# Kernel optimization log

Hardware: AMD Instinct MI355X
Metric: run time of the kernel (lower is better)

## Reference

```python
import jax, jax.numpy as jnp
import numpy as np

B, S, H, G, W = 4, 4096, 1024, 256, 8
CHUNK = 1024
NUM_HEADS = 4


def _ln(x, g, b, eps=1e-5):
    m = jnp.mean(x, axis=-1, keepdims=True)
    v = jnp.var(x, axis=-1, keepdims=True)
    return (x - m) / jnp.sqrt(v + eps) * g + b


def setup_inputs() -> dict:
    key = jax.random.key(0)
    ks = jax.random.split(key, 16)
    Hm = H // 2
    return {
        "x": jax.random.normal(ks[0], (B, S, H), dtype=jnp.float32),
        # wavelet params
        "mother_wavelets": jax.random.normal(ks[1], (1, W, H, 1), dtype=jnp.float32) * 0.02,
        "scales": jnp.ones((1, W, 1, 1), dtype=jnp.float32),
        # coeff_mixer: Linear(W,H/2) -> LN -> GELU -> Linear(H/2,H)  (weights stored as (in,out))
        "mix_w1": jax.random.normal(ks[2], (W, Hm), dtype=jnp.float32) * 0.02,
        "mix_b1": jnp.zeros((Hm,), dtype=jnp.float32),
        "mix_ln_g": jnp.ones((Hm,), dtype=jnp.float32),
        "mix_ln_b": jnp.zeros((Hm,), dtype=jnp.float32),
        "mix_w2": jax.random.normal(ks[3], (Hm, H), dtype=jnp.float32) * 0.02,
        "mix_b2": jnp.zeros((H,), dtype=jnp.float32),
        # attention (no bias)
        "wq": jax.random.normal(ks[4], (H, H), dtype=jnp.float32) * 0.02,
        "wk": jax.random.normal(ks[5], (H, H), dtype=jnp.float32) * 0.02,
        "wv": jax.random.normal(ks[6], (H, H), dtype=jnp.float32) * 0.02,
        "wo": jax.random.normal(ks[7], (H, H), dtype=jnp.float32) * 0.02,
        # output_proj: LN -> Linear(H, G)
        "out_ln_g": jnp.ones((H,), dtype=jnp.float32),
        "out_ln_b": jnp.zeros((H,), dtype=jnp.float32),
        "out_w": jax.random.normal(ks[8], (H, G), dtype=jnp.float32) * 0.02,
        "out_b": jnp.zeros((G,), dtype=jnp.float32),
    }


def reference(x, mother_wavelets, scales, mix_w1, mix_b1, mix_ln_g, mix_ln_b,
              mix_w2, mix_b2, wq, wk, wv, wo, out_ln_g, out_ln_b, out_w, out_b):
    b, s, h = x.shape
    nc = s // CHUNK  # chunks are independent -> fold into batch
    xc = x.reshape(b * nc, CHUNK, h)

    # wavelet coeffs: conv1d with kernel length == channels reduces to a dot product
    norm = jnp.sqrt(jnp.sum(mother_wavelets ** 2, axis=2, keepdims=True))
    kern = (mother_wavelets / jnp.maximum(norm, 1e-12)) * jax.nn.sigmoid(scales)
    kern = kern[0, :, :, 0]  # (W, H)
    coeffs = jnp.einsum('bsh,wh->bsw', xc, kern)  # (b*nc, L, W)

    # coeff mixer
    hid = _ln(coeffs @ mix_w1 + mix_b1, mix_ln_g, mix_ln_b)
    mixed = jax.nn.gelu(hid, approximate=False) @ mix_w2 + mix_b2  # (b*nc, L, H)

    # multi-head attention within each chunk (eval mode -> no causal mask)
    hd = h // NUM_HEADS
    def heads(t):
        return t.reshape(-1, CHUNK, NUM_HEADS, hd).transpose(0, 2, 1, 3)
    q, k, v = heads(mixed @ wq), heads(mixed @ wk), heads(mixed @ wv)
    scores = jnp.einsum('bhqd,bhkd->bhqk', q, k) * (hd ** -0.5)
    attn = jax.nn.softmax(scores, axis=-1)
    o = jnp.einsum('bhqk,bhkd->bhqd', attn, v)
    o = o.transpose(0, 2, 1, 3).reshape(-1, CHUNK, h) @ wo

    # output projection with residual
    y = _ln(o + mixed, out_ln_g, out_ln_b) @ out_w + out_b  # (b*nc, L, G)
    return y.reshape(b, s, -1)
```

## Files before the change

kernel.cpp:

```cpp
#include <hip/hip_runtime.h>
#include <hip/hip_bf16.h>

typedef __bf16 bf16;
typedef __bf16 bf16x4 __attribute__((ext_vector_type(4)));
typedef __bf16 bf16x8 __attribute__((ext_vector_type(8)));
typedef float f32x4 __attribute__((ext_vector_type(4)));
typedef unsigned short ushort8_t __attribute__((ext_vector_type(8)));
typedef unsigned int u32x2 __attribute__((ext_vector_type(2)));

#define GLOAD_LDS16(g, l)                                                      \
    __builtin_amdgcn_global_load_lds(                                          \
        (const __attribute__((address_space(1))) void*)(g),                    \
        (__attribute__((address_space(3))) void*)(l), 16, 0, 0)

#define LDS_ADDR(p) ((unsigned)(uintptr_t)(__attribute__((address_space(3))) void*)(p))

#define SBAR()                                                                 \
    do {                                                                       \
        __builtin_amdgcn_sched_barrier(0);                                     \
        __builtin_amdgcn_s_barrier();                                          \
        __builtin_amdgcn_sched_barrier(0);                                     \
    } while (0)


__global__ __launch_bounds__(256) void k_wavelet(const float* __restrict__ mw,
                                                 const float* __restrict__ sc,
                                                 float* __restrict__ kern) {
    int w = blockIdx.x;
    int tid = threadIdx.x;
    float s = 0.f;
    for (int h = tid; h < 1024; h += 256) { float v = mw[w * 1024 + h]; s += v * v; }
#pragma unroll
    for (int xm = 1; xm < 64; xm <<= 1) s += __shfl_xor(s, xm);
    __shared__ float red[4];
    if ((tid & 63) == 0) red[tid >> 6] = s;
    __syncthreads();
    float tot = red[0] + red[1] + red[2] + red[3];
    float inv = 1.f / fmaxf(sqrtf(tot), 1e-12f);
    float sg = 1.f / (1.f + __expf(-sc[w]));
    float m = inv * sg;
    for (int h = tid; h < 1024; h += 256) kern[w * 1024 + h] = mw[w * 1024 + h] * m;
}

__global__ __launch_bounds__(256) void k_coeffs(const float* __restrict__ x,
                                                const float* __restrict__ kern,
                                                float* __restrict__ coeffs) {
    __shared__ float kl[8 * 1024];
    int tid = threadIdx.x;
    for (int i = tid; i < 8192; i += 256) kl[i] = kern[i];
    __syncthreads();
    int wid = tid >> 6, lane = tid & 63;
    long row = (long)blockIdx.x * 4 + wid;
    float acc[8] = {0, 0, 0, 0, 0, 0, 0, 0};
    const float* xr = x + row * 1024;
    for (int i = 0; i < 16; i++) {
        float xv = xr[lane + i * 64];
#pragma unroll
        for (int w = 0; w < 8; w++) acc[w] += xv * kl[w * 1024 + lane + i * 64];
    }
#pragma unroll
    for (int xm = 1; xm < 64; xm <<= 1) {
#pragma unroll
        for (int w = 0; w < 8; w++) acc[w] += __shfl_xor(acc[w], xm);
    }
    if (lane == 0) {
#pragma unroll
        for (int w = 0; w < 8; w++) coeffs[row * 8 + w] = acc[w];
    }
}

__global__ __launch_bounds__(256) void k_mix1(const float* __restrict__ coeffs,
                                              const float* __restrict__ w1,
                                              const float* __restrict__ b1,
                                              const float* __restrict__ lng,
                                              const float* __restrict__ lnb,
                                              bf16* __restrict__ g) {
    long row = blockIdx.x;
    int tid = threadIdx.x;
    int wid = tid >> 6, lane = tid & 63;
    __shared__ float cf[8];
    __shared__ float red1[4], red2[4];
    if (tid < 8) cf[tid] = coeffs[row * 8 + tid];
    __syncthreads();
    float h0[2];
#pragma unroll
    for (int t = 0; t < 2; t++) {
        int j = tid + t * 256;
        float a = b1[j];
#pragma unroll
        for (int w = 0; w < 8; w++) a += cf[w] * w1[w * 512 + j];
        h0[t] = a;
    }
    float s1 = h0[0] + h0[1];
    float s2 = h0[0] * h0[0] + h0[1] * h0[1];
#pragma unroll
    for (int xm = 1; xm < 64; xm <<= 1) {
        s1 += __shfl_xor(s1, xm);
        s2 += __shfl_xor(s2, xm);
    }
    if (lane == 0) { red1[wid] = s1; red2[wid] = s2; }
    __syncthreads();
    s1 = red1[0] + red1[1] + red1[2] + red1[3];
    s2 = red2[0] + red2[1] + red2[2] + red2[3];
    float mean = s1 * (1.f / 512.f);
    float var = s2 * (1.f / 512.f) - mean * mean;
    float inv = rsqrtf(var + 1e-5f);
#pragma unroll
    for (int t = 0; t < 2; t++) {
        int j = tid + t * 256;
        float xn = (h0[t] - mean) * inv * lng[j] + lnb[j];
        float ge = 0.5f * xn * (1.f + erff(xn * 0.70710678118654752f));
        g[row * 512 + j] = (bf16)ge;
    }
}

__global__ void k_wtrans_all(const float* __restrict__ w2, const float* __restrict__ wq,
                             const float* __restrict__ wk, const float* __restrict__ wv,
                             const float* __restrict__ wo, const float* __restrict__ ow,
                             bf16* __restrict__ w2t, bf16* __restrict__ wqt,
                             bf16* __restrict__ wkt, bf16* __restrict__ wvt,
                             bf16* __restrict__ wot, bf16* __restrict__ owt) {
    long idx = (long)blockIdx.x * 256 + threadIdx.x;
    if (idx < 524288) {
        int kk = (int)(idx >> 10), n = (int)(idx & 1023);
        w2t[(long)n * 512 + kk] = (bf16)w2[idx];
    } else if (idx < 4718592) {
        long r = idx - 524288;
        int m = (int)(r >> 20);
        long q = r & 1048575;
        int kk = (int)(q >> 10), n = (int)(q & 1023);
        const float* src = (m == 0) ? wq : (m == 1) ? wk : (m == 2) ? wv : wo;
        bf16* dst = (m == 0) ? wqt : (m == 1) ? wkt : (m == 2) ? wvt : wot;
        dst[(long)n * 1024 + kk] = (bf16)src[q];
    } else {
        long r = idx - 4718592;
        int kk = (int)(r >> 8), n = (int)(r & 255);
        owt[(long)n * 1024 + kk] = (bf16)ow[r];
    }
}

enum { EPI_BF16 = 0, EPI_BF16_BIAS = 1, EPI_F32_BIAS = 2, EPI_VT = 3, EPI_F32 = 4 };

template <int EPI>
__global__ __launch_bounds__(512, 2) void k_gemm8p(const bf16* __restrict__ A,
                                                   const bf16* __restrict__ Bt,
                                                   const float* __restrict__ bias,
                                                   void* __restrict__ Cout,
                                                   int K, int lda, int ldb, int ldc,
                                                   float scale) {
    __shared__ bf16 As[2 * 2 * 128 * 64];
    __shared__ bf16 Bs[2 * 2 * 128 * 64];
    const int tid = threadIdx.x;
    const int wid = tid >> 6, lane = tid & 63;
    const int wr = wid >> 2, wc = wid & 3;
    const long m0 = (long)blockIdx.y * 256, n0 = (long)blockIdx.x * 256;
    f32x4 acc[8][4] = {};
    const int lr = lane & 15, gq = lane >> 4;
    const int l7 = lr & 7;

    const int srow = wid * 8 + (lane >> 3);
    const int sg = (lane & 7) ^ (lane >> 3);
    const bf16* aS = A + (m0 + srow) * lda + sg * 8;
    const bf16* bS = Bt + (n0 + srow) * ldb + sg * 8;

    auto stageA = [&](int t, int h) {
        bf16* d = As + (((t & 1) * 2 + h) * 128) * 64 + wid * 512;
        const long kq = (long)t << 6;
        GLOAAD_DUMMY:;
        GLOAD_LDS16(aS + (long)(h * 128) * lda + kq, d);
        GLOAD_LDS16(aS + (long)(h * 128 + 64) * lda + kq, d + 4096);
    };
    auto stageB = [&](int t, int h) {
        bf16* d = Bs + (((t & 1) * 2 + h) * 128) * 64 + wid * 512;
        const long kq = (long)t << 6;
        GLOAD_LDS16(bS + (long)(h * 128) * ldb + kq, d);
        GLOAD_LDS16(bS + (long)(h * 128 + 64) * ldb + kq, d + 4096);
    };

    bf16x8 bfr[4][2];
    auto ldB = [&](int b) {
#pragma unroll
        for (int j = 0; j < 4; j++)
#pragma unroll
            for (int kk = 0; kk < 2; kk++)
                bfr[j][kk] = *(const bf16x8*)&Bs[((b * 2 + (wc >> 1)) * 128 +
                                                 (wc & 1) * 64 + j * 16 + lr) * 64 +
                                                (((kk * 4 + gq) ^ l7) << 3)];
    };

    const int nt = K >> 6;
    const int niter = nt >> 1;

    stageA(0, 0); stageA(0, 1); stageB(0, 0); stageB(0, 1);
    stageB(1, 0); stageB(1, 1);
    asm volatile("s_waitcnt vmcnt(4)" ::: "memory");
    SBAR();

    for (int jit = 0; jit < niter - 1; ++jit) {
        const int T = jit << 1;
#pragma unroll
        for (int tp = 0; tp < 2; ++tp) {
#pragma unroll
            for (int q = 0; q < 4; ++q) {
                bf16x8 af[2][2];
                if (q == 0) ldB(tp);
#pragma unroll
                for (int ii = 0; ii < 2; ii++)
#pragma unroll
                    for (int kk = 0; kk < 2; kk++)
                        af[ii][kk] = *(const bf16x8*)&As[((tp * 2 + wr) * 128 +
                                                         (q * 2 + ii) * 16 + lr) * 64 +
                                                        (((kk * 4 + gq) ^ l7) << 3)];
                if (tp == 0) {
                    if (q == 0) stageA(T + 1, 0);
                    else if (q == 1) stageA(T + 1, 1);
                    else if (q == 2) stageB(T + 2, 0);
                    else stageB(T + 2, 1);
                } else {
                    if (q == 0) stageA(T + 2, 0);
                    else if (q == 1) stageA(T + 2, 1);
                    else if (q == 2) stageB(T + 3, 0);
                    else stageB(T + 3, 1);
                }
                if (q == 3) asm volatile("s_waitcnt vmcnt(4)" ::: "memory");
                SBAR();
                asm volatile("s_waitcnt lgkmcnt(0)" ::: "memory");
                __builtin_amdgcn_s_setprio(1);
#pragma unroll
                for (int ii = 0; ii < 2; ii++)
#pragma unroll
                    for (int j = 0; j < 4; j++) {
                        acc[q * 2 + ii][j] = __builtin_amdgcn_mfma_f32_16x16x32_bf16(
                            af[ii][0], bfr[j][0], acc[q * 2 + ii][j], 0, 0, 0);
                        acc[q * 2 + ii][j] = __builtin_amdgcn_mfma_f32_16x16x32_bf16(
                            af[ii][1], bfr[j][1], acc[q * 2 + ii][j], 0, 0, 0);
                    }
                __builtin_amdgcn_s_setprio(0);
                SBAR();
            }
        }
    }
    {
        const int T = nt - 2;
#pragma unroll
        for (int tp = 0; tp < 2; ++tp) {
#pragma unroll
            for (int q = 0; q < 4; ++q) {
                bf16x8 af[2][2];
                if (q == 0) ldB(tp);
#pragma unroll
                for (int ii = 0; ii < 2; ii++)
#pragma unroll
                    for (int kk = 0; kk < 2; kk++)
                        af[ii][kk] = *(const bf16x8*)&As[((tp * 2 + wr) * 128 +
                                                         (q * 2 + ii) * 16 + lr) * 64 +
                                                        (((kk * 4 + gq) ^ l7) << 3)];
                if (tp == 0 && q == 0) stageA(T + 1, 0);
                if (tp == 0 && q == 1) stageA(T + 1, 1);
                if (tp == 0 && q == 3) asm volatile("s_waitcnt vmcnt(0)" ::: "memory");
                SBAR();
                asm volatile("s_waitcnt lgkmcnt(0)" ::: "memory");
                __builtin_amdgcn_s_setprio(1);
#pragma unroll
                for (int ii = 0; ii < 2; ii++)
#pragma unroll
                    for (int j = 0; j < 4; j++) {
                        acc[q * 2 + ii][j] = __builtin_amdgcn_mfma_f32_16x16x32_bf16(
                            af[ii][0], bfr[j][0], acc[q * 2 + ii][j], 0, 0, 0);
                        acc[q * 2 + ii][j] = __builtin_amdgcn_mfma_f32_16x16x32_bf16(
                            af[ii][1], bfr[j][1], acc[q * 2 + ii][j], 0, 0, 0);
                    }
                __builtin_amdgcn_s_setprio(0);
                SBAR();
            }
        }
    }

    const int r0 = (lane >> 4) << 2;
#pragma unroll
    for (int i = 0; i < 8; i++) {
#pragma unroll
        for (int j = 0; j < 4; j++) {
#pragma unroll
            for (int e = 0; e < 4; e++) {
                long m = m0 + wr * 128 + i * 16 + r0 + e;
                long n = n0 + wc * 64 + j * 16 + lr;
                float v = acc[i][j][e] * scale;
                if constexpr (EPI == EPI_BF16_BIAS || EPI == EPI_F32_BIAS) v += bias[n];
                if constexpr (EPI == EPI_F32_BIAS || EPI == EPI_F32) {
                    ((float*)Cout)[m * ldc + n] = v;
                } else if constexpr (EPI == EPI_VT) {
                    long c = m >> 10, s = m & 1023, h = n >> 8, d = n & 255;
                    ((bf16*)Cout)[(((c << 2) + h) << 18) + (d << 10) + s] = (bf16)v;
                } else {
                    ((bf16*)Cout)[m * ldc + n] = (bf16)v;
                }
            }
        }
    }
}

template <int EPI>
__global__ __launch_bounds__(256) void k_gemm(const bf16* __restrict__ A,
                                              const bf16* __restrict__ Bt,
                                              const float* __restrict__ bias,
                                              void* __restrict__ Cout,
                                              int M, int N, int K,
                                              int lda, int ldb, int ldc, float scale) {
    __shared__ bf16 As[128 * 32];
    __shared__ bf16 Bs[128 * 32];
    int tid = threadIdx.x;
    int wid = tid >> 6, lane = tid & 63;
    int wr = wid >> 1, wc = wid & 1;
    long m0 = (long)blockIdx.y * 128, n0 = (long)blockIdx.x * 128;
    f32x4 acc[4][4] = {};
    const int lr = lane & 15, ko = (lane >> 4) << 3;

    const int srow = wid * 32 + (lane >> 2);
    const int scol = (lane & 3) << 3;
    const bf16* a0 = A + (m0 + srow) * lda + scol;
    const bf16* a1 = A + (m0 + srow + 16) * lda + scol;
    const bf16* b0 = Bt + (n0 + srow) * ldb + scol;
    const bf16* b1 = Bt + (n0 + srow + 16) * ldb + scol;
    bf16* la0 = As + wid * 1024;
    bf16* la1 = As + wid * 1024 + 512;
    bf16* lb0 = Bs + wid * 1024;
    bf16* lb1 = Bs + wid * 1024 + 512;

    for (int k0 = 0; k0 < K; k0 += 32) {
        GLOAD_LDS16(a0 + k0, la0);
        GLOAD_LDS16(a1 + k0, la1);
        GLOAD_LDS16(b0 + k0, lb0);
        GLOAD_LDS16(b1 + k0, lb1);
        __syncthreads();
        bf16x8 af[4], bfr[4];
#pragma unroll
        for (int i = 0; i < 4; i++)
            af[i] = *(const bf16x8*)&As[(wr * 64 + i * 16 + lr) * 32 + ko];
#pragma unroll
        for (int i = 0; i < 4; i++)
            bfr[i] = *(const bf16x8*)&Bs[(wc * 64 + i * 16 + lr) * 32 + ko];
#pragma unroll
        for (int i = 0; i < 4; i++) {
#pragma unroll
            for (int j = 0; j < 4; j++)
                acc[i][j] = __builtin_amdgcn_mfma_f32_16x16x32_bf16(af[i], bfr[j], acc[i][j], 0, 0, 0);
        }
        __syncthreads();
    }
    const int r0 = (lane >> 4) << 2;
#pragma unroll
    for (int i = 0; i < 4; i++) {
#pragma unroll
        for (int j = 0; j < 4; j++) {
#pragma unroll
            for (int e = 0; e < 4; e++) {
                long m = m0 + wr * 64 + i * 16 + r0 + e;
                long n = n0 + wc * 64 + j * 16 + lr;
                float v = acc[i][j][e] * scale;
                if constexpr (EPI == EPI_BF16_BIAS || EPI == EPI_F32_BIAS) v += bias[n];
                if constexpr (EPI == EPI_F32_BIAS || EPI == EPI_F32) {
                    ((float*)Cout)[m * ldc + n] = v;
                } else if constexpr (EPI == EPI_VT) {
                    long c = m >> 10, s = m & 1023, h = n >> 8, d = n & 255;
                    ((bf16*)Cout)[(((c << 2) + h) << 18) + (d << 10) + s] = (bf16)v;
                } else {
                    ((bf16*)Cout)[m * ldc + n] = (bf16)v;
                }
            }
        }
    }
}

__global__ __launch_bounds__(512, 2) void k_attn(const bf16* __restrict__ q,
                                                 const bf16* __restrict__ k,
                                                 const bf16* __restrict__ vt,
                                                 bf16* __restrict__ ao) {
    __shared__ __align__(16) bf16 smem[2 * 16384 + 2 * 16384 + 8192];
    bf16* Ks = smem;
    bf16* Vs = smem + 32768;
    bf16* Ps = smem + 65536;
    int tid = threadIdx.x;
    int wid = tid >> 6, lane = tid & 63;
    int c = blockIdx.x, h = blockIdx.y, q0 = blockIdx.z * 128;
    const int lr = lane & 15, gq = lane >> 4, ko = gq << 3;
    const int l7 = lr & 7;

    const int krw = wid * 2 + (lane >> 5);
    const int kg = (lane & 31) ^ (krw & 7);
    const bf16* ksrc = k + ((long)c << 10) * 1024 + h * 256 + kg * 8;
    const int vrw = wid * 8 + ((lane >> 3) & 7);
    const int vg = (lane & 7) ^ ((lane >> 3) & 7);
    const bf16* vsrc = vt + ((long)(c * 4 + h) << 18) + vg * 8;

    long qrow = ((long)c << 10) + q0 + wid * 16 + lr;
    bf16x8 qf[8];
#pragma unroll
    for (int kk = 0; kk < 8; kk++)
        qf[kk] = *(const bf16x8*)&q[qrow * 1024 + h * 256 + kk * 32 + ko];

    f32x4 oacc[16] = {};
    float m_run[4] = {-1e30f, -1e30f, -1e30f, -1e30f};
    float l_run[4] = {0.f, 0.f, 0.f, 0.f};

    bf16* PT = Ps + (wid << 10);
    const unsigned pva = LDS_ADDR(&PT[(gq << 7) + lr]);

#pragma unroll
    for (int i = 0; i < 4; i++) {
        GLOAD_LDS16(ksrc + (long)(i * 16 + krw) * 1024, Ks + i * 4096 + wid * 512);
        GLOAD_LDS16(vsrc + (long)(i * 64 + vrw) * 1024, Vs + i * 4096 + wid * 512);
    }
    __syncthreads();
    int buf = 0;
    for (int t = 0; t < 16; t++) {
        if (t < 15) {
            const int kb = (t + 1) << 6;
            const int ob = (buf ^ 1) << 14;
#pragma unroll
            for (int i = 0; i < 4; i++) {
                GLOAD_LDS16(ksrc + (long)(kb + i * 16 + krw) * 1024, Ks + ob + i * 4096 + wid * 512);
                GLOAD_LDS16(vsrc + (long)(i * 64 + vrw) * 1024 + kb, Vs + ob + i * 4096 + wid * 512);
            }
        }
        const bf16* Kc = Ks + (buf << 14);
        const bf16* Vc = Vs + (buf << 14);
        f32x4 s[4] = {};
        __builtin_amdgcn_s_setprio(1);
#pragma unroll
        for (int kk = 0; kk < 8; kk++) {
#pragma unroll
            for (int n = 0; n < 4; n++)
                s[n] = __builtin_amdgcn_mfma_f32_16x16x32_bf16(
                    qf[kk],
                    *(const bf16x8*)&Kc[((n * 16 + lr) << 8) + ((((kk << 2) + gq) ^ l7) << 3)],
                    s[n], 0, 0, 0);
        }
        __builtin_amdgcn_s_setprio(0);
        float mx[4];
#pragma unroll
        for (int e = 0; e < 4; e++)
            mx[e] = fmaxf(fmaxf(s[0][e], s[1][e]), fmaxf(s[2][e], s[3][e]));
#pragma unroll
        for (int xm = 1; xm < 16; xm <<= 1) {
#pragma unroll
            for (int e = 0; e < 4; e++) mx[e] = fmaxf(mx[e], __shfl_xor(mx[e], xm));
        }
        bool need = (mx[0] > m_run[0] + 8.f) || (mx[1] > m_run[1] + 8.f) ||
                    (mx[2] > m_run[2] + 8.f) || (mx[3] > m_run[3] + 8.f);
        if (__any(need)) {
#pragma unroll
            for (int e = 0; e < 4; e++) {
                float mn = fmaxf(m_run[e], mx[e]);
                float al = __expf(m_run[e] - mn);
                m_run[e] = mn;
                l_run[e] *= al;
#pragma unroll
                for (int f = 0; f < 16; f++) oacc[f][e] *= al;
            }
        }
        float rs[4] = {0.f, 0.f, 0.f, 0.f};
#pragma unroll
        for (int n = 0; n < 4; n++) {
#pragma unroll
            for (int e = 0; e < 4; e++) {
                float p = __expf(s[n][e] - m_run[e]);
                s[n][e] = p;
                rs[e] += p;
            }
        }
#pragma unroll
        for (int xm = 1; xm < 16; xm <<= 1) {
#pragma unroll
            for (int e = 0; e < 4; e++) rs[e] += __shfl_xor(rs[e], xm);
        }
#pragma unroll
        for (int e = 0; e < 4; e++) l_run[e] += rs[e];
#pragma unroll
        for (int n = 0; n < 4; n++) {
            bf16x4 pv = {(bf16)s[n][0], (bf16)s[n][1], (bf16)s[n][2], (bf16)s[n][3]};
            *(bf16x4*)&PT[((n * 16 + lr) << 4) + (gq << 2)] = pv;
        }
        asm volatile("s_waitcnt lgkmcnt(0)" ::: "memory");
        u32x2 t0, t1, t2, t3;
        asm volatile("ds_read_b64_tr_b16 %0, %1" : "=v"(t0) : "v"(pva));
        asm volatile("ds_read_b64_tr_b16 %0, %1 offset:128" : "=v"(t1) : "v"(pva));
        asm volatile("ds_read_b64_tr_b16 %0, %1 offset:1024" : "=v"(t2) : "v"(pva));
        asm volatile("ds_read_b64_tr_b16 %0, %1 offset:1152" : "=v"(t3) : "v"(pva));
        asm volatile("s_waitcnt lgkmcnt(0)" ::: "memory");
        __builtin_amdgcn_sched_barrier(0);
        union { u32x2 u[2]; bf16x8 v; } p0, p1;
        p0.u[0] = t0; p0.u[1] = t1;
        p1.u[0] = t2; p1.u[1] = t3;
        const bf16x8 pf0 = p0.v, pf1 = p1.v;
        __builtin_amdgcn_s_setprio(1);
#pragma unroll
        for (int n2 = 0; n2 < 16; n2++) {
            const int vrow = (n2 * 16 + lr) << 6;
            const int vswz = gq ^ l7;
            oacc[n2] = __builtin_amdgcn_mfma_f32_16x16x32_bf16(
                pf0, *(const bf16x8*)&Vc[vrow + (vswz << 3)], oacc[n2], 0, 0, 0);
            oacc[n2] = __builtin_amdgcn_mfma_f32_16x16x32_bf16(
                pf1, *(const bf16x8*)&Vc[vrow + ((vswz ^ 4) << 3)], oacc[n2], 0, 0, 0);
        }
        __builtin_amdgcn_s_setprio(0);
        __syncthreads();
        buf ^= 1;
    }
#pragma unroll
    for (int n2 = 0; n2 < 16; n2++) {
#pragma unroll
        for (int e = 0; e < 4; e++) {
            long row = ((long)c << 10) + q0 + wid * 16 + (gq << 2) + e;
            long col = ((long)h << 8) + n2 * 16 + lr;
            ao[row * 1024 + col] = (bf16)(oacc[n2][e] / l_run[e]);
        }
    }
}

__global__ __launch_bounds__(256) void k_outln(const bf16* __restrict__ o,
                                               const bf16* __restrict__ mixed,
                                               const float* __restrict__ g,
                                               const float* __restrict__ b,
                                               bf16* __restrict__ t) {
    long row = blockIdx.x;
    int tid = threadIdx.x;
    int wid = tid >> 6, lane = tid & 63;
    __shared__ float red1[4], red2[4];
    float x[4];
    const bf16* orow = o + row * 1024;
    const bf16* mrow = mixed + row * 1024;
    bf16x4 ov = *(const bf16x4*)&orow[tid * 4];
    bf16x4 mv = *(const bf16x4*)&mrow[tid * 4];
#pragma unroll
    for (int i = 0; i < 4; i++) x[i] = (float)ov[i] + (float)mv[i];
    float s1 = x[0] + x[1] + x[2] + x[3];
    float s2 = x[0] * x[0] + x[1] * x[1] + x[2] * x[2] + x[3] * x[3];
#pragma unroll
    for (int xm = 1; xm < 64; xm <<= 1) {
        s1 += __shfl_xor(s1, xm);
        s2 += __shfl_xor(s2, xm);
    }
    if (lane == 0) { red1[wid] = s1; red2[wid] = s2; }
    __syncthreads();
    s1 = red1[0] + red1[1] + red1[2] + red1[3];
    s2 = red2[0] + red2[1] + red2[2] + red2[3];
    float mean = s1 * (1.f / 1024.f);
    float var = s2 * (1.f / 1024.f) - mean * mean;
    float inv = rsqrtf(var + 1e-5f);
#pragma unroll
    for (int i = 0; i < 4; i++) {
        int j = tid * 4 + i;
        t[row * 1024 + j] = (bf16)((x[i] - mean) * inv * g[j] + b[j]);
    }
}

extern "C" void kernel_launch(void* const* d_in, const int* in_sizes, int n_in,
                              void* d_out, int out_size, void* d_ws, size_t ws_size,
                              hipStream_t stream) {
    const float* x   = (const float*)d_in[0];
    const float* mw  = (const float*)d_in[1];
    const float* sc  = (const float*)d_in[2];
    const float* w1  = (const float*)d_in[3];
    const float* b1  = (const float*)d_in[4];
    const float* lng1 = (const float*)d_in[5];
    const float* lnb1 = (const float*)d_in[6];
    const float* w2  = (const float*)d_in[7];
    const float* b2  = (const float*)d_in[8];
    const float* wq  = (const float*)d_in[9];
    const float* wk  = (const float*)d_in[10];
    const float* wv  = (const float*)d_in[11];
    const float* wo  = (const float*)d_in[12];
    const float* lng2 = (const float*)d_in[13];
    const float* lnb2 = (const float*)d_in[14];
    const float* ow  = (const float*)d_in[15];
    const float* ob  = (const float*)d_in[16];

    char* p = (char*)d_ws;
    auto take = [&](size_t bytes) {
        char* r = p;
        p += (bytes + 255) & ~(size_t)255;
        return r;
    };
    const size_t M = 16384;
    float* kern   = (float*)take(8 * 1024 * sizeof(float));
    float* coeffs = (float*)take(M * 8 * sizeof(float));
    bf16* g       = (bf16*)take(M * 512 * 2);
    bf16* mixed   = (bf16*)take(M * 1024 * 2);
    bf16* qb      = (bf16*)take(M * 1024 * 2 * 2);
    bf16* kb2     = qb + M * 1024;
    bf16* obf     = qb;
    bf16* vtb     = (bf16*)take(M * 1024 * 2);
    bf16* tb      = vtb;
    bf16* aob     = (bf16*)take(M * 1024 * 2);
    bf16* w2t     = (bf16*)take((size_t)1024 * 512 * 2);
    bf16* wqt     = (bf16*)take((size_t)1024 * 1024 * 2);
    bf16* wkt     = (bf16*)take((size_t)1024 * 1024 * 2);
    bf16* wvt     = (bf16*)take((size_t)1024 * 1024 * 2);
    bf16* wot     = (bf16*)take((size_t)1024 * 1024 * 2);
    bf16* owt     = (bf16*)take((size_t)256 * 1024 * 2);

    k_wavelet<<<8, 256, 0, stream>>>(mw, sc, kern);
    k_coeffs<<<4096, 256, 0, stream>>>(x, kern, coeffs);
    k_mix1<<<16384, 256, 0, stream>>>(coeffs, w1, b1, lng1, lnb1, g);

    k_wtrans_all<<<19456, 256, 0, stream>>>(w2, wq, wk, wv, wo, ow,
                                            w2t, wqt, wkt, wvt, wot, owt);

    k_gemm8p<EPI_BF16_BIAS><<<dim3(4, 64), 512, 0, stream>>>(
        g, w2t, b2, mixed, 512, 512, 512, 1024, 1.f);
    k_gemm8p<EPI_BF16><<<dim3(4, 64), 512, 0, stream>>>(
        mixed, wqt, nullptr, qb, 1024, 1024, 1024, 1024, 0.0625f);
    k_gemm8p<EPI_BF16><<<dim3(4, 64), 512, 0, stream>>>(
        mixed, wkt, nullptr, kb2, 1024, 1024, 1024, 1024, 1.f);
    k_gemm8p<EPI_VT><<<dim3(4, 64), 512, 0, stream>>>(
        mixed, wvt, nullptr, vtb, 1024, 1024, 1024, 1024, 1.f);
    k_attn<<<dim3(16, 4, 8), 512, 0, stream>>>(qb, kb2, vtb, aob);
    k_gemm8p<EPI_BF16><<<dim3(4, 64), 512, 0, stream>>>(
        aob, wot, nullptr, obf, 1024, 1024, 1024, 1024, 1.f);
    k_outln<<<16384, 256, 0, stream>>>(obf, mixed, lng2, lnb2, tb);
    k_gemm<EPI_F32_BIAS><<<dim3(2, 128), 256, 0, stream>>>(
        tb, owt, ob, d_out, 16384, 256, 1024, 1024, 1024, 256, 1.f);
}
```

Baseline: 431.4 us.

## Fuse Q/K/V projections into one GEMM launch; read V from global in attention

```diff
diff --git a/kernel.cpp b/kernel.cpp
--- a/kernel.cpp
+++ b/kernel.cpp
@@ -139,13 +139,15 @@
     }
 }
 
-enum { EPI_BF16 = 0, EPI_BF16_BIAS = 1, EPI_F32_BIAS = 2, EPI_VT = 3, EPI_F32 = 4 };
+enum { EPI_BF16 = 0, EPI_BF16_BIAS = 1, EPI_F32_BIAS = 2, EPI_VT = 3, EPI_F32 = 4, EPI_QKV = 5 };
 
 template <int EPI>
 __global__ __launch_bounds__(512, 2) void k_gemm8p(const bf16* __restrict__ A,
                                                    const bf16* __restrict__ Bt,
                                                    const float* __restrict__ bias,
                                                    void* __restrict__ Cout,
+                                                   void* __restrict__ CoutK,
+                                                   void* __restrict__ CoutV,
                                                    int K, int lda, int ldb, int ldc,
                                                    float scale) {
     __shared__ bf16 As[2 * 2 * 128 * 64];
@@ -166,7 +168,6 @@
     auto stageA = [&](int t, int h) {
         bf16* d = As + (((t & 1) * 2 + h) * 128) * 64 + wid * 512;
         const long kq = (long)t << 6;
-        GLOAAD_DUMMY:;
         GLOAD_LDS16(aS + (long)(h * 128) * lda + kq, d);
         GLOAD_LDS16(aS + (long)(h * 128 + 64) * lda + kq, d + 4096);
     };
@@ -292,6 +293,17 @@
                 } else if constexpr (EPI == EPI_VT) {
                     long c = m >> 10, s = m & 1023, h = n >> 8, d = n & 255;
                     ((bf16*)Cout)[(((c << 2) + h) << 18) + (d << 10) + s] = (bf16)v;
+                } else if constexpr (EPI == EPI_QKV) {
+                    int which = (int)(n >> 10);
+                    long ncol = n & 1023;
+                    if (which == 0) {
+                        ((bf16*)Cout)[m * 1024 + ncol] = (bf16)(v * 0.0625f);
+                    } else if (which == 1) {
+                        ((bf16*)CoutK)[m * 1024 + ncol] = (bf16)v;
+                    } else {
+                        long c = m >> 10, s = m & 1023, h = ncol >> 8, d = ncol & 255;
+                        ((bf16*)CoutV)[(((c << 2) + h) << 18) + (d << 10) + s] = (bf16)v;
+                    }
                 } else {
                     ((bf16*)Cout)[m * ldc + n] = (bf16)v;
                 }
@@ -361,9 +373,6 @@
                 if constexpr (EPI == EPI_BF16_BIAS || EPI == EPI_F32_BIAS) v += bias[n];
                 if constexpr (EPI == EPI_F32_BIAS || EPI == EPI_F32) {
                     ((float*)Cout)[m * ldc + n] = v;
-                } else if constexpr (EPI == EPI_VT) {
-                    long c = m >> 10, s = m & 1023, h = n >> 8, d = n & 255;
-                    ((bf16*)Cout)[(((c << 2) + h) << 18) + (d << 10) + s] = (bf16)v;
                 } else {
                     ((bf16*)Cout)[m * ldc + n] = (bf16)v;
                 }
@@ -376,10 +385,9 @@
                                                  const bf16* __restrict__ k,
                                                  const bf16* __restrict__ vt,
                                                  bf16* __restrict__ ao) {
-    __shared__ __align__(16) bf16 smem[2 * 16384 + 2 * 16384 + 8192];
+    __shared__ __align__(16) bf16 smem[2 * 16384 + 8192];
     bf16* Ks = smem;
-    bf16* Vs = smem + 32768;
-    bf16* Ps = smem + 65536;
+    bf16* Ps = smem + 32768;
     int tid = threadIdx.x;
     int wid = tid >> 6, lane = tid & 63;
     int c = blockIdx.x, h = blockIdx.y, q0 = blockIdx.z * 128;
@@ -389,9 +397,7 @@
     const int krw = wid * 2 + (lane >> 5);
     const int kg = (lane & 31) ^ (krw & 7);
     const bf16* ksrc = k + ((long)c << 10) * 1024 + h * 256 + kg * 8;
-    const int vrw = wid * 8 + ((lane >> 3) & 7);
-    const int vg = (lane & 7) ^ ((lane >> 3) & 7);
-    const bf16* vsrc = vt + ((long)(c * 4 + h) << 18) + vg * 8;
+    const bf16* vbase = vt + ((long)(c * 4 + h) << 18);
 
     long qrow = ((long)c << 10) + q0 + wid * 16 + lr;
     bf16x8 qf[8];
@@ -407,10 +413,8 @@
     const unsigned pva = LDS_ADDR(&PT[(gq << 7) + lr]);
 
 #pragma unroll
-    for (int i = 0; i < 4; i++) {
+    for (int i = 0; i < 4; i++)
         GLOAD_LDS16(ksrc + (long)(i * 16 + krw) * 1024, Ks + i * 4096 + wid * 512);
-        GLOAD_LDS16(vsrc + (long)(i * 64 + vrw) * 1024, Vs + i * 4096 + wid * 512);
-    }
     __syncthreads();
     int buf = 0;
     for (int t = 0; t < 16; t++) {
@@ -418,13 +422,11 @@
             const int kb = (t + 1) << 6;
             const int ob = (buf ^ 1) << 14;
 #pragma unroll
-            for (int i = 0; i < 4; i++) {
+            for (int i = 0; i < 4; i++)
                 GLOAD_LDS16(ksrc + (long)(kb + i * 16 + krw) * 1024, Ks + ob + i * 4096 + wid * 512);
-                GLOAD_LDS16(vsrc + (long)(i * 64 + vrw) * 1024 + kb, Vs + ob + i * 4096 + wid * 512);
-            }
         }
         const bf16* Kc = Ks + (buf << 14);
-        const bf16* Vc = Vs + (buf << 14);
+        const bf16* vgl = vbase + ((long)t << 6);
         f32x4 s[4] = {};
         __builtin_amdgcn_s_setprio(1);
 #pragma unroll
@@ -496,12 +498,11 @@
         __builtin_amdgcn_s_setprio(1);
 #pragma unroll
         for (int n2 = 0; n2 < 16; n2++) {
-            const int vrow = (n2 * 16 + lr) << 6;
-            const int vswz = gq ^ l7;
-            oacc[n2] = __builtin_amdgcn_mfma_f32_16x16x32_bf16(
-                pf0, *(const bf16x8*)&Vc[vrow + (vswz << 3)], oacc[n2], 0, 0, 0);
-            oacc[n2] = __builtin_amdgcn_mfma_f32_16x16x32_bf16(
-                pf1, *(const bf16x8*)&Vc[vrow + ((vswz ^ 4) << 3)], oacc[n2], 0, 0, 0);
+            const long vo = (long)(n2 * 16 + lr) * 1024 + ko;
+            const bf16x8 vlo = *(const bf16x8*)&vgl[vo];
+            const bf16x8 vhi = *(const bf16x8*)&vgl[vo + 32];
+            oacc[n2] = __builtin_amdgcn_mfma_f32_16x16x32_bf16(pf0, vlo, oacc[n2], 0, 0, 0);
+            oacc[n2] = __builtin_amdgcn_mfma_f32_16x16x32_bf16(pf1, vhi, oacc[n2], 0, 0, 0);
         }
         __builtin_amdgcn_s_setprio(0);
         __syncthreads();
@@ -608,16 +609,12 @@
                                             w2t, wqt, wkt, wvt, wot, owt);
 
     k_gemm8p<EPI_BF16_BIAS><<<dim3(4, 64), 512, 0, stream>>>(
-        g, w2t, b2, mixed, 512, 512, 512, 1024, 1.f);
-    k_gemm8p<EPI_BF16><<<dim3(4, 64), 512, 0, stream>>>(
-        mixed, wqt, nullptr, qb, 1024, 1024, 1024, 1024, 0.0625f);
-    k_gemm8p<EPI_BF16><<<dim3(4, 64), 512, 0, stream>>>(
-        mixed, wkt, nullptr, kb2, 1024, 1024, 1024, 1024, 1.f);
-    k_gemm8p<EPI_VT><<<dim3(4, 64), 512, 0, stream>>>(
-        mixed, wvt, nullptr, vtb, 1024, 1024, 1024, 1024, 1.f);
+        g, w2t, b2, mixed, nullptr, nullptr, 512, 512, 512, 1024, 1.f);
+    k_gemm8p<EPI_QKV><<<dim3(12, 64), 512, 0, stream>>>(
+        mixed, wqt, nullptr, qb, kb2, vtb, 1024, 1024, 1024, 1024, 1.f);
     k_attn<<<dim3(16, 4, 8), 512, 0, stream>>>(qb, kb2, vtb, aob);
     k_gemm8p<EPI_BF16><<<dim3(4, 64), 512, 0, stream>>>(
-        aob, wot, nullptr, obf, 1024, 1024, 1024, 1024, 1.f);
+        aob, wot, nullptr, obf, nullptr, nullptr, 1024, 1024, 1024, 1024, 1.f);
     k_outln<<<16384, 256, 0, stream>>>(obf, mixed, lng2, lnb2, tb);
     k_gemm<EPI_F32_BIAS><<<dim3(2, 128), 256, 0, stream>>>(
         tb, owt, ob, d_out, 16384, 256, 1024, 1024, 1024, 256, 1.f);
```

Result: slower. 658.0 us (+52.5%).
